# Performance work log

Measured on AMD Instinct MI355X. Metric: run time of the kernel, lower is better.

Reference implementation:

```python
import jax, jax.numpy as jnp
import numpy as np
import math

B, L, D_MODEL, H = 8, 3072, 1024, 16
E = D_MODEL // H                      # d_keys = d_values = 64
FACTOR = 1
TOP_K = int(FACTOR * math.log(L))     # = 8 delay taps


def setup_inputs() -> dict:
    key = jax.random.key(0)
    ks = jax.random.split(key, 11)
    s = 0.02
    return {
        "queries": jax.random.normal(ks[0], (B, L, D_MODEL), jnp.float32),
        "keys":    jax.random.normal(ks[1], (B, L, D_MODEL), jnp.float32),
        "values":  jax.random.normal(ks[2], (B, L, D_MODEL), jnp.float32),
        "Wq": jax.random.normal(ks[3], (D_MODEL, D_MODEL), jnp.float32) * s,
        "bq": jnp.zeros((D_MODEL,), jnp.float32),
        "Wk": jax.random.normal(ks[4], (D_MODEL, D_MODEL), jnp.float32) * s,
        "bk": jnp.zeros((D_MODEL,), jnp.float32),
        "Wv": jax.random.normal(ks[5], (D_MODEL, D_MODEL), jnp.float32) * s,
        "bv": jnp.zeros((D_MODEL,), jnp.float32),
        "Wo": jax.random.normal(ks[6], (D_MODEL, D_MODEL), jnp.float32) * s,
        "bo": jnp.zeros((D_MODEL,), jnp.float32),
    }


def reference(queries, keys, values, Wq, bq, Wk, bk, Wv, bv, Wo, bo):
    # Q/K/V projections -> [B, L, H, E]
    q = (queries @ Wq + bq).reshape(B, L, H, E)
    k = (keys    @ Wk + bk).reshape(B, L, H, E)
    v = (values  @ Wv + bv).reshape(B, L, H, E)

    # -> [B, H, E, L], correlate along time via FFT
    qh = q.transpose(0, 2, 3, 1)
    kh = k.transpose(0, 2, 3, 1)
    vh = v.transpose(0, 2, 3, 1)
    qf = jnp.fft.rfft(qh, axis=-1)
    kf = jnp.fft.rfft(kh, axis=-1)
    corr = jnp.fft.irfft(qf * jnp.conj(kf), n=L, axis=-1)  # [B, H, E, L]

    # per-batch top-k delay selection on head/channel-averaged correlation
    mean_value = corr.mean(axis=(1, 2))                    # [B, L]
    weights, delay = jax.lax.top_k(mean_value, TOP_K)      # [B, K]
    tmp_corr = jax.nn.softmax(weights, axis=-1)            # [B, K]

    # time-delay aggregation: circular gather per selected delay, weighted sum
    init_index = jnp.arange(L)
    agg = jnp.zeros_like(vh)
    for i in range(TOP_K):  # small static loop over top-k taps
        idx = (init_index[None, :] + delay[:, i:i + 1]) % L            # [B, L]
        idx4 = jnp.broadcast_to(idx[:, None, None, :], vh.shape)       # [B,H,E,L]
        pattern = jnp.take_along_axis(vh, idx4, axis=-1)
        agg = agg + pattern * tmp_corr[:, i][:, None, None, None]

    # back to [B, L, H*E], output projection
    V = agg.transpose(0, 3, 1, 2).reshape(B, L, H * E)
    return V @ Wo + bo
```

## Files before the change

kernel.cpp:

```cpp
#include <hip/hip_runtime.h>
#include <math.h>

#define BSZ 8
#define LEN 3072
#define DM 1024
#define TOPK 8

typedef __attribute__((ext_vector_type(8))) short short8;
typedef __attribute__((ext_vector_type(4))) float f32x4;

__device__ __forceinline__ unsigned short f2bf(float x) {
    unsigned int u = __builtin_bit_cast(unsigned int, x);
    u += 0x7fffu + ((u >> 16) & 1u);
    return (unsigned short)(u >> 16);
}
__device__ __forceinline__ float bf2f(unsigned short h) {
    unsigned int u = ((unsigned int)h) << 16;
    return __builtin_bit_cast(float, u);
}
__device__ __forceinline__ void gl_lds16(const void* g, void* l) {
    __builtin_amdgcn_global_load_lds(
        (const __attribute__((address_space(1))) unsigned int*)g,
        (__attribute__((address_space(3))) unsigned int*)l, 16, 0, 0);
}

#define GBM 128
#define GBN 128
#define GBK 16

__global__ __launch_bounds__(256) void gemm_f32_sk(const float* __restrict__ A,
    const float* __restrict__ B, float* __restrict__ P, int M, int N, int K)
{
    __shared__ float As[GBK][GBM];
    __shared__ float Bs[GBK][GBN];
    const int tid = threadIdx.x;
    const int tx = tid & 15, ty = tid >> 4;
    const size_t m0 = (size_t)blockIdx.y * GBM;
    const size_t n0 = (size_t)blockIdx.x * GBN;
    const int ksl = K >> 2;
    const int kb = blockIdx.z * ksl, ke = kb + ksl;
    const int arow = tid >> 2, acol = (tid & 3) << 2;
    const int brow = tid >> 5, bcol = (tid & 31) << 2;

    float acc[8][8];
#pragma unroll
    for (int i = 0; i < 8; i++)
#pragma unroll
        for (int j = 0; j < 8; j++) acc[i][j] = 0.f;

    const float* Ap0 = A + (m0 + arow) * (size_t)K + acol;
    const float* Ap1 = A + (m0 + arow + 64) * (size_t)K + acol;
    const float* Bp0 = B + (size_t)brow * N + n0 + bcol;
    const float* Bp1 = B + (size_t)(brow + 8) * N + n0 + bcol;

    for (int k0 = kb; k0 < ke; k0 += GBK) {
        float4 a0 = *(const float4*)(Ap0 + k0);
        float4 a1 = *(const float4*)(Ap1 + k0);
        float4 b0 = *(const float4*)(Bp0 + (size_t)k0 * N);
        float4 b1 = *(const float4*)(Bp1 + (size_t)k0 * N);
        __syncthreads();
        As[acol + 0][arow] = a0.x; As[acol + 1][arow] = a0.y;
        As[acol + 2][arow] = a0.z; As[acol + 3][arow] = a0.w;
        As[acol + 0][arow + 64] = a1.x; As[acol + 1][arow + 64] = a1.y;
        As[acol + 2][arow + 64] = a1.z; As[acol + 3][arow + 64] = a1.w;
        *(float4*)&Bs[brow][bcol] = b0;
        *(float4*)&Bs[brow + 8][bcol] = b1;
        __syncthreads();
#pragma unroll
        for (int kk = 0; kk < GBK; kk++) {
            float av[8], bv[8];
            *(float4*)&av[0] = *(const float4*)&As[kk][ty * 8];
            *(float4*)&av[4] = *(const float4*)&As[kk][ty * 8 + 4];
            *(float4*)&bv[0] = *(const float4*)&Bs[kk][tx * 8];
            *(float4*)&bv[4] = *(const float4*)&Bs[kk][tx * 8 + 4];
#pragma unroll
            for (int i = 0; i < 8; i++)
#pragma unroll
                for (int j = 0; j < 8; j++)
                    acc[i][j] = fmaf(av[i], bv[j], acc[i][j]);
        }
    }
    float* Pz = P + (size_t)blockIdx.z * M * N;
#pragma unroll
    for (int i = 0; i < 8; i++) {
        size_t row = m0 + (size_t)(ty * 8 + i);
        float* Cp = Pz + row * N + n0 + tx * 8;
#pragma unroll
        for (int j = 0; j < 8; j++) Cp[j] = acc[i][j];
    }
}

__global__ __launch_bounds__(256) void reduce4_f32(const float* __restrict__ P,
                                                   float* __restrict__ C, int n)
{
    int i = (blockIdx.x * 256 + threadIdx.x) * 4;
    if (i >= n) return;
    float4 a = *(const float4*)(P + i);
    float4 b = *(const float4*)(P + (size_t)n + i);
    float4 c = *(const float4*)(P + 2 * (size_t)n + i);
    float4 d = *(const float4*)(P + 3 * (size_t)n + i);
    float4 o = {a.x + b.x + c.x + d.x, a.y + b.y + c.y + d.y,
                a.z + b.z + c.z + d.z, a.w + b.w + c.w + d.w};
    *(float4*)(C + i) = o;
}

__device__ __forceinline__ void xcd_tile(int& bx, int& by) {
    int nbx = gridDim.x, nby = gridDim.y;
    int nwg = nbx * nby;
    int flat = by * nbx + bx;
    if (!(nwg & 7)) {
        int sw = (flat & 7) * (nwg >> 3) + (flat >> 3);
        bx = sw % nbx;
        by = sw / nbx;
    }
}

__global__ __launch_bounds__(256) void gemm_split_zT(
    const unsigned short* __restrict__ Khi, const unsigned short* __restrict__ Klo,
    const unsigned short* __restrict__ AhiT, const unsigned short* __restrict__ AloT,
    const float* __restrict__ bias, float* __restrict__ zT, int M, int N, int K)
{
    __shared__ unsigned short Ah[128 * 32];
    __shared__ unsigned short Al[128 * 32];
    __shared__ unsigned short Bh[128 * 32];
    __shared__ unsigned short Bl[128 * 32];
    const int tid = threadIdx.x;
    const int lane = tid & 63;
    const int wv = tid >> 6;
    const int wm = wv >> 1, wn = wv & 1;
    const int l16 = lane & 15, quad = lane >> 4;
    int bx = blockIdx.x, by = blockIdx.y;
    xcd_tile(bx, by);
    const size_t m0 = (size_t)by * 128;
    const size_t n0 = (size_t)bx * 128;

    const int s0 = tid, s1 = tid + 256;
    const size_t oA0 = (m0 + (s0 >> 2)) * (size_t)K + (s0 & 3) * 8;
    const size_t oA1 = (m0 + (s1 >> 2)) * (size_t)K + (s1 & 3) * 8;
    const size_t oB0 = (n0 + (s0 >> 2)) * (size_t)K + (s0 & 3) * 8;
    const size_t oB1 = (n0 + (s1 >> 2)) * (size_t)K + (s1 & 3) * 8;

    f32x4 acc[4][4];
#pragma unroll
    for (int i = 0; i < 4; i++)
#pragma unroll
        for (int j = 0; j < 4; j++) acc[i][j] = (f32x4){0.f, 0.f, 0.f, 0.f};

    for (int k0 = 0; k0 < K; k0 += 32) {
        __syncthreads();
        gl_lds16(Khi + oA0 + k0, &Ah[s0 * 8]);
        gl_lds16(Khi + oA1 + k0, &Ah[s1 * 8]);
        gl_lds16(Klo + oA0 + k0, &Al[s0 * 8]);
        gl_lds16(Klo + oA1 + k0, &Al[s1 * 8]);
        gl_lds16(AhiT + oB0 + k0, &Bh[s0 * 8]);
        gl_lds16(AhiT + oB1 + k0, &Bh[s1 * 8]);
        gl_lds16(AloT + oB0 + k0, &Bl[s0 * 8]);
        gl_lds16(AloT + oB1 + k0, &Bl[s1 * 8]);
        __syncthreads();
        short8 ah[4], al[4], bh[4], bl[4];
#pragma unroll
        for (int mi = 0; mi < 4; mi++) {
            int off = (wm * 64 + mi * 16 + l16) * 32 + quad * 8;
            ah[mi] = *(const short8*)&Ah[off];
            al[mi] = *(const short8*)&Al[off];
        }
#pragma unroll
        for (int ni = 0; ni < 4; ni++) {
            int off = (wn * 64 + ni * 16 + l16) * 32 + quad * 8;
            bh[ni] = *(const short8*)&Bh[off];
            bl[ni] = *(const short8*)&Bl[off];
        }
#pragma unroll
        for (int mi = 0; mi < 4; mi++)
#pragma unroll
            for (int ni = 0; ni < 4; ni++) {
                acc[mi][ni] = __builtin_amdgcn_mfma_f32_16x16x32_bf16(
                    ah[mi], bh[ni], acc[mi][ni], 0, 0, 0);
                acc[mi][ni] = __builtin_amdgcn_mfma_f32_16x16x32_bf16(
                    ah[mi], bl[ni], acc[mi][ni], 0, 0, 0);
                acc[mi][ni] = __builtin_amdgcn_mfma_f32_16x16x32_bf16(
                    al[mi], bh[ni], acc[mi][ni], 0, 0, 0);
            }
    }

    const int b = (int)(m0 / LEN);
    const int t0 = (int)(m0 % LEN);
#pragma unroll
    for (int mi = 0; mi < 4; mi++) {
#pragma unroll
        for (int ni = 0; ni < 4; ni++) {
            int c = (int)n0 + wn * 64 + ni * 16 + l16;
            int t = t0 + wm * 64 + mi * 16 + quad * 4;
            float bb = bias[c];
            float* zp = zT + ((size_t)b * DM + c) * LEN + t;
#pragma unroll
            for (int r = 0; r < 4; r++) zp[r] = acc[mi][ni][r] + bb;
        }
    }
}

__global__ __launch_bounds__(256) void gemm_bf16(const unsigned short* __restrict__ A,
    const unsigned short* __restrict__ Bt, const float* __restrict__ bias,
    void* __restrict__ C, int M, int N, int K, int cmode)
{
    __shared__ unsigned short As[128 * 32];
    __shared__ unsigned short Bs[128 * 32];
    const int tid = threadIdx.x;
    const int lane = tid & 63;
    const int wv = tid >> 6;
    const int wm = wv >> 1, wn = wv & 1;
    const int l16 = lane & 15, quad = lane >> 4;
    int bx = blockIdx.x, by = blockIdx.y;
    xcd_tile(bx, by);
    const size_t m0 = (size_t)by * 128;
    const size_t n0 = (size_t)bx * 128;

    const int s0 = tid, s1 = tid + 256;
    const unsigned short* gA0 = A + (m0 + (s0 >> 2)) * (size_t)K + (s0 & 3) * 8;
    const unsigned short* gA1 = A + (m0 + (s1 >> 2)) * (size_t)K + (s1 & 3) * 8;
    const unsigned short* gB0 = Bt + (n0 + (s0 >> 2)) * (size_t)K + (s0 & 3) * 8;
    const unsigned short* gB1 = Bt + (n0 + (s1 >> 2)) * (size_t)K + (s1 & 3) * 8;
    unsigned short* lA0 = &As[s0 * 8];
    unsigned short* lA1 = &As[s1 * 8];
    unsigned short* lB0 = &Bs[s0 * 8];
    unsigned short* lB1 = &Bs[s1 * 8];

    f32x4 acc[4][4];
#pragma unroll
    for (int i = 0; i < 4; i++)
#pragma unroll
        for (int j = 0; j < 4; j++) acc[i][j] = (f32x4){0.f, 0.f, 0.f, 0.f};

    for (int k0 = 0; k0 < K; k0 += 32) {
        __syncthreads();
        gl_lds16(gA0 + k0, lA0);
        gl_lds16(gA1 + k0, lA1);
        gl_lds16(gB0 + k0, lB0);
        gl_lds16(gB1 + k0, lB1);
        __syncthreads();
        short8 af[4], bf[4];
#pragma unroll
        for (int mi = 0; mi < 4; mi++)
            af[mi] = *(const short8*)&As[(wm * 64 + mi * 16 + l16) * 32 + quad * 8];
#pragma unroll
        for (int ni = 0; ni < 4; ni++)
            bf[ni] = *(const short8*)&Bs[(wn * 64 + ni * 16 + l16) * 32 + quad * 8];
#pragma unroll
        for (int mi = 0; mi < 4; mi++)
#pragma unroll
            for (int ni = 0; ni < 4; ni++)
                acc[mi][ni] = __builtin_amdgcn_mfma_f32_16x16x32_bf16(
                    af[mi], bf[ni], acc[mi][ni], 0, 0, 0);
    }

#pragma unroll
    for (int mi = 0; mi < 4; mi++) {
#pragma unroll
        for (int ni = 0; ni < 4; ni++) {
            int gm = (int)m0 + wm * 64 + mi * 16 + quad * 4;
            int gn = (int)n0 + wn * 64 + ni * 16 + l16;
            float bb = bias ? bias[gn] : 0.f;
#pragma unroll
            for (int r = 0; r < 4; r++) {
                float v = acc[mi][ni][r] + bb;
                if (cmode == 0)
                    ((float*)C)[(size_t)(gm + r) * N + gn] = v;
                else
                    ((unsigned short*)C)[(size_t)(gm + r) * N + gn] = f2bf(v);
            }
        }
    }
}

__global__ __launch_bounds__(256) void transpose_bld(const float* __restrict__ in,
                                                     float* __restrict__ out)
{
    __shared__ float tile[32][33];
    int b = blockIdx.z;
    int d0 = blockIdx.x * 32, t0 = blockIdx.y * 32;
    int tx = threadIdx.x & 31, ty = threadIdx.x >> 5;
    const float* ip = in + (size_t)b * LEN * DM;
    float* op = out + (size_t)b * DM * LEN;
#pragma unroll
    for (int r = 0; r < 4; r++)
        tile[ty * 4 + r][tx] = ip[(size_t)(t0 + ty * 4 + r) * DM + d0 + tx];
    __syncthreads();
#pragma unroll
    for (int r = 0; r < 4; r++)
        op[(size_t)(d0 + ty * 4 + r) * LEN + t0 + tx] = tile[tx][ty * 4 + r];
}

__global__ __launch_bounds__(256) void transpose_1024(const float* __restrict__ in,
                                                      float* __restrict__ out)
{
    __shared__ float tile[32][33];
    int bx = blockIdx.x & 31, by = blockIdx.x >> 5;
    int tx = threadIdx.x & 31, tq = threadIdx.x >> 5;
#pragma unroll
    for (int r = 0; r < 4; r++)
        tile[tq * 4 + r][tx] = in[(size_t)(by * 32 + tq * 4 + r) * 1024 + bx * 32 + tx];
    __syncthreads();
#pragma unroll
    for (int r = 0; r < 4; r++)
        out[(size_t)(bx * 32 + tq * 4 + r) * 1024 + by * 32 + tx] = tile[tx][tq * 4 + r];
}

__global__ __launch_bounds__(256) void transpose_w_bf16(const float* __restrict__ in,
                                                        unsigned short* __restrict__ out)
{
    __shared__ float tile[32][33];
    int bx = blockIdx.x & 31, by = blockIdx.x >> 5;
    int tx = threadIdx.x & 31, tq = threadIdx.x >> 5;
#pragma unroll
    for (int r = 0; r < 4; r++)
        tile[tq * 4 + r][tx] = in[(size_t)(by * 32 + tq * 4 + r) * 1024 + bx * 32 + tx];
    __syncthreads();
#pragma unroll
    for (int r = 0; r < 4; r++)
        out[(size_t)(bx * 32 + tq * 4 + r) * 1024 + by * 32 + tx] = f2bf(tile[tx][tq * 4 + r]);
}

__global__ __launch_bounds__(256) void transpose_w_split(const float* __restrict__ in,
    unsigned short* __restrict__ hi, unsigned short* __restrict__ lo)
{
    __shared__ float tile[32][33];
    int bx = blockIdx.x & 31, by = blockIdx.x >> 5;
    int tx = threadIdx.x & 31, tq = threadIdx.x >> 5;
#pragma unroll
    for (int r = 0; r < 4; r++)
        tile[tq * 4 + r][tx] = in[(size_t)(by * 32 + tq * 4 + r) * 1024 + bx * 32 + tx];
    __syncthreads();
#pragma unroll
    for (int r = 0; r < 4; r++) {
        float x = tile[tx][tq * 4 + r];
        unsigned short h = f2bf(x);
        unsigned short l = f2bf(x - bf2f(h));
        size_t o = (size_t)(bx * 32 + tq * 4 + r) * 1024 + by * 32 + tx;
        hi[o] = h; lo[o] = l;
    }
}

__global__ __launch_bounds__(256) void split_bf16(const float* __restrict__ in,
    unsigned short* __restrict__ hi, unsigned short* __restrict__ lo, size_t n)
{
    size_t i = ((size_t)blockIdx.x * 256 + threadIdx.x) * 4;
    if (i >= n) return;
    float4 v = *(const float4*)(in + i);
    ushort4 h, l;
    h.x = f2bf(v.x); l.x = f2bf(v.x - bf2f(h.x));
    h.y = f2bf(v.y); l.y = f2bf(v.y - bf2f(h.y));
    h.z = f2bf(v.z); l.z = f2bf(v.z - bf2f(h.z));
    h.w = f2bf(v.w); l.w = f2bf(v.w - bf2f(h.w));
    *(ushort4*)(hi + i) = h;
    *(ushort4*)(lo + i) = l;
}

__global__ __launch_bounds__(256) void conv_bf16(const float* __restrict__ in,
                                                 unsigned short* __restrict__ out, size_t n)
{
    size_t i = ((size_t)blockIdx.x * 256 + threadIdx.x) * 4;
    if (i >= n) return;
    float4 v = *(const float4*)(in + i);
    ushort4 o;
    o.x = f2bf(v.x); o.y = f2bf(v.y); o.z = f2bf(v.z); o.w = f2bf(v.w);
    *(ushort4*)(out + i) = o;
}

__global__ __launch_bounds__(256) void bz_kernel(const float* __restrict__ bk,
    const float* __restrict__ WqT, float* __restrict__ bz)
{
    int j = blockIdx.x * 256 + threadIdx.x;
    float s = 0.f;
    for (int d = 0; d < 1024; d++) s = fmaf(bk[d], WqT[(size_t)d * 1024 + j], s);
    bz[j] = s;
}

__device__ __forceinline__ int swz(int i) { return i ^ ((i >> 4) & 15); }

__device__ __forceinline__ float2 cmul(float2 a, float2 b) {
    return make_float2(a.x * b.x - a.y * b.y, a.x * b.y + a.y * b.x);
}

struct TwRegs {
    float2 wA[5], w2[5], w1[4], w2c[4];
};

__device__ __forceinline__ void make_tw(TwRegs& T, int tid)
{
    const float TWO_PI = 6.28318530717958647692f;
#pragma unroll
    for (int si = 0; si < 5; si++) {
        int s = si * 2;
        int a = (tid >> s) << s;
        float sv, cv; sincosf(-TWO_PI * (float)a / 1024.f, &sv, &cv);
        T.wA[si] = make_float2(cv, sv);
        T.w2[si] = make_float2(cv * cv - sv * sv, 2.f * cv * sv);
    }
#pragma unroll
    for (int j = 0; j < 4; j++) {
        int k2 = tid + (j << 8);
        float sv, cv; sincosf(-TWO_PI * (float)k2 / 3072.f, &sv, &cv);
        T.w1[j] = make_float2(cv, sv);
        T.w2c[j] = make_float2(cv * cv - sv * sv, 2.f * cv * sv);
    }
}

__device__ __forceinline__ void fft3072_r4(float2* __restrict__ bufA,
                                           float2* __restrict__ bufB,
                                           const TwRegs& T, int tid)
{
    float2* src = bufA;
    float2* dst = bufB;
#pragma unroll
    for (int s = 0; s < 10; s += 2) {
        const int st = 1 << s;
        const int q = tid & (st - 1);
        const int p = tid >> s;
        const float2 wA = T.wA[s >> 1];
        const float2 w2 = T.w2[s >> 1];
        const int io = q + (p << (s + 2));
#pragma unroll
        for (int k = 0; k < 3; k++) {
            const int base = k << 10;
            float2 a1 = src[swz(base + tid)];
            float2 a2 = src[swz(base + tid + 256)];
            float2 b1 = src[swz(base + tid + 512)];
            float2 b2 = src[swz(base + tid + 768)];
            float2 uA0 = make_float2(a1.x + b1.x, a1.y + b1.y);
            float2 d1  = make_float2(a1.x - b1.x, a1.y - b1.y);
            float2 uA1 = cmul(d1, wA);
            float2 uB0 = make_float2(a2.x + b2.x, a2.y + b2.y);
            float2 d2  = make_float2(a2.x - b2.x, a2.y - b2.y);
            float2 e   = cmul(d2, wA);
            float2 uB1 = make_float2(e.y, -e.x);
            float2 o0 = make_float2(uA0.x + uB0.x, uA0.y + uB0.y);
            float2 o1 = make_float2(uA1.x + uB1.x, uA1.y + uB1.y);
            float2 e2 = make_float2(uA0.x - uB0.x, uA0.y - uB0.y);
            float2 e3 = make_float2(uA1.x - uB1.x, uA1.y - uB1.y);
            dst[swz(base + io)] = o0;
            dst[swz(base + io + st)] = o1;
            dst[swz(base + io + 2 * st)] = cmul(e2, w2);
            dst[swz(base + io + 3 * st)] = cmul(e3, w2);
        }
        __syncthreads();
        float2* t = src; src = dst; dst = t;
    }
    const float OMR = -0.5f, OMI = -0.86602540378443864676f;
#pragma unroll
    for (int j = 0; j < 4; j++) {
        int k2 = tid + (j << 8);
        float2 y0 = src[swz(k2)];
        float2 y1 = src[swz(1024 + k2)];
        float2 y2 = src[swz(2048 + k2)];
        float2 w1 = T.w1[j];
        float2 w2c = T.w2c[j];
        float2 u1 = cmul(y1, w1);
        float2 u2 = cmul(y2, w2c);
        dst[swz(k2)] = make_float2(y0.x + u1.x + u2.x, y0.y + u1.y + u2.y);
        dst[swz(1024 + k2)] = make_float2(
            y0.x + (OMR * u1.x - OMI * u1.y) + (OMR * u2.x + OMI * u2.y),
            y0.y + (OMR * u1.y + OMI * u1.x) + (OMR * u2.y - OMI * u2.x));
        dst[swz(2048 + k2)] = make_float2(
            y0.x + (OMR * u1.x + OMI * u1.y) + (OMR * u2.x - OMI * u2.y),
            y0.y + (OMR * u1.y - OMI * u1.x) + (OMR * u2.y + OMI * u2.x));
    }
    __syncthreads();
}

#define SLAB 3104

__global__ __launch_bounds__(256) void fft_corr(const float* __restrict__ qT,
    const float* __restrict__ zT, float* __restrict__ Spart)
{
    __shared__ float2 bufA[3072], bufB[3072];
    const int tid = threadIdx.x;
    const int b = blockIdx.x >> 6;
    const int c0 = (blockIdx.x & 63) << 4;
    TwRegs T;
    make_tw(T, tid);
    float pR[6], pI[6];
#pragma unroll
    for (int j = 0; j < 6; j++) { pR[j] = 0.f; pI[j] = 0.f; }
    float eR = 0.f, eI = 0.f;

    const float* qp = qT + ((size_t)b * DM + c0) * LEN;
    const float* zp = zT + ((size_t)b * DM + c0) * LEN;
    float qv[12], zv[12];
#pragma unroll
    for (int j = 0; j < 12; j++) {
        int t = tid + (j << 8);
        qv[j] = qp[t]; zv[j] = zp[t];
    }

    for (int ci = 0; ci < 16; ci++) {
#pragma unroll
        for (int j = 0; j < 12; j++) {
            int t = tid + (j << 8);
            int t1 = t % 3, t2 = t / 3;
            bufA[swz(t1 * 1024 + t2)] = make_float2(qv[j], zv[j]);
        }
        if (ci < 15) {
            const float* qn = qp + (size_t)(ci + 1) * LEN;
            const float* zn = zp + (size_t)(ci + 1) * LEN;
#pragma unroll
            for (int j = 0; j < 12; j++) {
                int t = tid + (j << 8);
                qv[j] = qn[t]; zv[j] = zn[t];
            }
        }
        __syncthreads();
        fft3072_r4(bufA, bufB, T, tid);
#pragma unroll
        for (int j = 0; j < 6; j++) {
            int f = tid + (j << 8);
            int fc = (f == 0) ? 0 : 3072 - f;
            float2 Wf = bufA[swz(f)];
            float2 Wc = bufA[swz(fc)];
            float WcI = -Wc.y;
            float qR = 0.5f * (Wf.x + Wc.x), qI = 0.5f * (Wf.y + WcI);
            float dR = Wf.x - Wc.x, dI = Wf.y - WcI;
            float zR = 0.5f * dI, zI = -0.5f * dR;
            pR[j] += qR * zR + qI * zI;
            pI[j] += qI * zR - qR * zI;
        }
        if (tid == 0) {
            float2 Wf = bufA[swz(1536)];
            eR += Wf.x * Wf.y;
        }
        __syncthreads();
    }
    float2* Pb = (float2*)(Spart + (size_t)blockIdx.x * SLAB);
#pragma unroll
    for (int j = 0; j < 6; j++) {
        int f = tid + (j << 8);
        Pb[f] = make_float2(pR[j], pI[j]);
    }
    if (tid == 0) Pb[1536] = make_float2(eR, eI);
}

__global__ __launch_bounds__(256) void reduce_S(const float* __restrict__ Spart,
                                                float* __restrict__ S)
{
    int g = blockIdx.x * 256 + threadIdx.x;
    if (g >= BSZ * 3074) return;
    int b = g / 3074, r = g - b * 3074;
    const float* p = Spart + (size_t)(b * 64) * SLAB + r;
    float s = 0.f;
#pragma unroll 8
    for (int k = 0; k < 64; k++) s += p[(size_t)k * SLAB];
    S[(size_t)b * 6144 + r] = s;
}

__global__ __launch_bounds__(256) void ifft_mean(const float* __restrict__ S,
                                                 float* __restrict__ mv)
{
    __shared__ float2 bufA[3072], bufB[3072];
    const int tid = threadIdx.x;
    const int b = blockIdx.x;
    TwRegs T;
    make_tw(T, tid);
    for (int t = tid; t < 3072; t += 256) {
        int tt = (t <= 1536) ? t : 3072 - t;
        float sR = S[((size_t)b * 3072 + tt) * 2 + 0];
        float sI = S[((size_t)b * 3072 + tt) * 2 + 1];
        float im = (t > 1536) ? sI : -sI;
        int t1 = t % 3, t2 = t / 3;
        bufA[swz(t1 * 1024 + t2)] = make_float2(sR, im);
    }
    __syncthreads();
    fft3072_r4(bufA, bufB, T, tid);
    const float scale = 1.f / (3072.f * 1024.f);
    for (int t = tid; t < 3072; t += 256)
        mv[(size_t)b * 3072 + t] = bufA[swz(t)].x * scale;
}

__global__ __launch_bounds__(256) void topk_softmax(const float* __restrict__ mv,
    float* __restrict__ wout, int* __restrict__ dout)
{
    const int b = blockIdx.x, tid = threadIdx.x;
    __shared__ float v[3072];
    __shared__ float rv[256];
    __shared__ int   ri[256];
    __shared__ float topv[TOPK];
    __shared__ int   topi[TOPK];
    for (int t = tid; t < 3072; t += 256) v[t] = mv[(size_t)b * 3072 + t];
    __syncthreads();
    for (int it = 0; it < TOPK; it++) {
        float best = -3.0e38f; int bi = 0;
        for (int t = tid; t < 3072; t += 256) {
            float x = v[t];
            if (x > best) { best = x; bi = t; }
        }
        rv[tid] = best; ri[tid] = bi;
        __syncthreads();
        for (int off = 128; off > 0; off >>= 1) {
            if (tid < off) {
                float ov = rv[tid + off]; int oi = ri[tid + off];
                if (ov > rv[tid] || (ov == rv[tid] && oi < ri[tid])) {
                    rv[tid] = ov; ri[tid] = oi;
                }
            }
            __syncthreads();
        }
        if (tid == 0) { topv[it] = rv[0]; topi[it] = ri[0]; v[ri[0]] = -3.0e38f; }
        __syncthreads();
    }
    if (tid == 0) {
        float m = topv[0];
        float e[TOPK]; float ssum = 0.f;
        for (int i = 0; i < TOPK; i++) { e[i] = expf(topv[i] - m); ssum += e[i]; }
        for (int i = 0; i < TOPK; i++) {
            wout[b * TOPK + i] = e[i] / ssum;
            dout[b * TOPK + i] = topi[i];
        }
    }
}

__global__ __launch_bounds__(256) void agg_bf16(const unsigned short* __restrict__ V,
    const float* __restrict__ w, const int* __restrict__ d,
    unsigned short* __restrict__ agg)
{
    size_t gid = (size_t)blockIdx.x * 256 + threadIdx.x;
    int c8 = (int)(gid & 127);
    size_t rest = gid >> 7;
    int t = (int)(rest % LEN);
    int b = (int)(rest / LEN);
    float acc[8];
#pragma unroll
    for (int j = 0; j < 8; j++) acc[j] = 0.f;
#pragma unroll
    for (int i = 0; i < TOPK; i++) {
        float wi = w[b * TOPK + i];
        int r = t + d[b * TOPK + i];
        if (r >= LEN) r -= LEN;
        const unsigned short* vp = V + ((size_t)b * LEN + r) * DM + c8 * 8;
        uint4 raw = *(const uint4*)vp;
        unsigned int uu[4] = {raw.x, raw.y, raw.z, raw.w};
#pragma unroll
        for (int k = 0; k < 4; k++) {
            acc[2 * k]     = fmaf(wi, bf2f((unsigned short)(uu[k] & 0xffff)), acc[2 * k]);
            acc[2 * k + 1] = fmaf(wi, bf2f((unsigned short)(uu[k] >> 16)), acc[2 * k + 1]);
        }
    }
    unsigned int ou[4];
#pragma unroll
    for (int k = 0; k < 4; k++)
        ou[k] = (unsigned int)f2bf(acc[2 * k]) | ((unsigned int)f2bf(acc[2 * k + 1]) << 16);
    uint4 o = {ou[0], ou[1], ou[2], ou[3]};
    *(uint4*)(agg + gid * 8) = o;
}

extern "C" void kernel_launch(void* const* d_in, const int* in_sizes, int n_in,
                              void* d_out, int out_size, void* d_ws, size_t ws_size,
                              hipStream_t stream)
{
    const float* queries = (const float*)d_in[0];
    const float* keys    = (const float*)d_in[1];
    const float* values  = (const float*)d_in[2];
    const float* Wq = (const float*)d_in[3];
    const float* Wk = (const float*)d_in[5];
    const float* bk = (const float*)d_in[6];
    const float* Wv = (const float*)d_in[7];
    const float* bv = (const float*)d_in[8];
    const float* Wo = (const float*)d_in[9];
    const float* bo = (const float*)d_in[10];
    float* out = (float*)d_out;

    char* ws = (char*)d_ws;
    size_t off = 0;
    auto alloc = [&](size_t bytes) -> char* {
        char* p = ws + off;
        off += (bytes + 255) & ~(size_t)255;
        return p;
    };
    const size_t BLD = (size_t)BSZ * LEN * DM;
    float* WqT  = (float*)alloc((size_t)1024 * 1024 * 4);
    float* Amat = (float*)alloc((size_t)1024 * 1024 * 4);
    unsigned short* AhiT = (unsigned short*)alloc((size_t)1024 * 1024 * 2);
    unsigned short* AloT = (unsigned short*)alloc((size_t)1024 * 1024 * 2);
    float* bz   = (float*)alloc(1024 * 4);
    float* S    = (float*)alloc((size_t)BSZ * 3072 * 2 * 4);
    float* mv   = (float*)alloc((size_t)BSZ * 3072 * 4);
    float* wsm  = (float*)alloc(BSZ * TOPK * 4);
    int*   dly  = (int*)alloc(BSZ * TOPK * 4);
    unsigned short* WvT = (unsigned short*)alloc((size_t)1024 * 1024 * 2);
    unsigned short* WoT = (unsigned short*)alloc((size_t)1024 * 1024 * 2);
    char* bigA = alloc(BLD * 4);
    char* bigB = alloc(BLD * 4);
    unsigned short* khi = (unsigned short*)bigA;
    unsigned short* klo = (unsigned short*)(bigA + BLD * 2);
    float* qT = (float*)bigA;
    float* zT = (float*)bigB;
    float* Apart = (float*)bigB;
    unsigned short* vb16 = (unsigned short*)bigA;
    unsigned short* aggb = (unsigned short*)(bigA + BLD * 2);
    unsigned short* Vb   = (unsigned short*)bigB;
    float* Spart = WqT;

    const int BL = BSZ * LEN;

    transpose_1024<<<1024, 256, 0, stream>>>(Wq, WqT);
    gemm_f32_sk<<<dim3(8, 8, 4), 256, 0, stream>>>(Wk, WqT, Apart, 1024, 1024, 1024);
    reduce4_f32<<<1024, 256, 0, stream>>>(Apart, Amat, 1024 * 1024);
    bz_kernel<<<4, 256, 0, stream>>>(bk, WqT, bz);
    transpose_w_split<<<1024, 256, 0, stream>>>(Amat, AhiT, AloT);
    split_bf16<<<(int)((BLD / 4 + 255) / 256), 256, 0, stream>>>(keys, khi, klo, BLD);
    gemm_split_zT<<<dim3(8, 192), 256, 0, stream>>>(khi, klo, AhiT, AloT, bz, zT,
                                                    BL, 1024, 1024);
    transpose_bld<<<dim3(32, 96, 8), 256, 0, stream>>>(queries, qT);
    fft_corr<<<BSZ * 64, 256, 0, stream>>>(qT, zT, Spart);
    reduce_S<<<(BSZ * 3074 + 255) / 256, 256, 0, stream>>>(Spart, S);
    ifft_mean<<<BSZ, 256, 0, stream>>>(S, mv);
    topk_softmax<<<BSZ, 256, 0, stream>>>(mv, wsm, dly);

    conv_bf16<<<(int)((BLD / 4 + 255) / 256), 256, 0, stream>>>(values, vb16, BLD);
    transpose_w_bf16<<<1024, 256, 0, stream>>>(Wv, WvT);
    transpose_w_bf16<<<1024, 256, 0, stream>>>(Wo, WoT);
    gemm_bf16<<<dim3(8, 192), 256, 0, stream>>>(vb16, WvT, bv, Vb, BL, 1024, 1024, 1);
    agg_bf16<<<(int)(((size_t)BL * 128) / 256), 256, 0, stream>>>(Vb, wsm, dly, aggb);
    gemm_bf16<<<dim3(8, 192), 256, 0, stream>>>(aggb, WoT, bo, out, BL, 1024, 1024, 0);
}
```

Before: 891.1 us.

## Unify GEMMs into triple-buffered swizzled pipeline and rebalance FFT block split

Replaces the split-bf16 and plain bf16 GEMM kernels with one templated kernel that triple-buffers LDS tiles using async global-to-LDS loads. It waits on the vmcnt counter instead of issuing two full barriers per k-step, and XOR-swizzles the LDS layout to avoid bank conflicts. The split-precision GEMM is recast as three sequential K-phases (hi*hi, hi*lo, lo*hi) over the same pipeline. The FFT correlation work is also redistributed from 64 to 96 blocks per batch so more blocks fill the GPU, at the cost of more partial slabs for the reduction to sum.

```diff
diff --git a/kernel.cpp b/kernel.cpp
--- a/kernel.cpp
+++ b/kernel.cpp
@@ -115,15 +115,14 @@
     }
 }
 
-__global__ __launch_bounds__(256) void gemm_split_zT(
-    const unsigned short* __restrict__ Khi, const unsigned short* __restrict__ Klo,
-    const unsigned short* __restrict__ AhiT, const unsigned short* __restrict__ AloT,
-    const float* __restrict__ bias, float* __restrict__ zT, int M, int N, int K)
-{
-    __shared__ unsigned short Ah[128 * 32];
-    __shared__ unsigned short Al[128 * 32];
-    __shared__ unsigned short Bh[128 * 32];
-    __shared__ unsigned short Bl[128 * 32];
+template<int KMODE, int CMODE>
+__global__ __launch_bounds__(256, 3) void gemm_pipe(
+    const unsigned short* __restrict__ A0, const unsigned short* __restrict__ A1,
+    const unsigned short* __restrict__ B0, const unsigned short* __restrict__ B1,
+    const float* __restrict__ bias, void* __restrict__ C, int M, int N, int NT)
+{
+    __shared__ unsigned short Ab[3][128 * 32];
+    __shared__ unsigned short Bb[3][128 * 32];
     const int tid = threadIdx.x;
     const int lane = tid & 63;
     const int wv = tid >> 6;
@@ -135,10 +134,41 @@
     const size_t n0 = (size_t)bx * 128;
 
     const int s0 = tid, s1 = tid + 256;
-    const size_t oA0 = (m0 + (s0 >> 2)) * (size_t)K + (s0 & 3) * 8;
-    const size_t oA1 = (m0 + (s1 >> 2)) * (size_t)K + (s1 & 3) * 8;
-    const size_t oB0 = (n0 + (s0 >> 2)) * (size_t)K + (s0 & 3) * 8;
-    const size_t oB1 = (n0 + (s1 >> 2)) * (size_t)K + (s1 & 3) * 8;
+    const int g0 = ((s0 & 3) ^ ((s0 >> 3) & 3)) * 8;
+    const int g1 = ((s1 & 3) ^ ((s1 >> 3) & 3)) * 8;
+    const size_t oA0 = (m0 + (s0 >> 2)) * 1024 + g0;
+    const size_t oA1 = (m0 + (s1 >> 2)) * 1024 + g1;
+    const size_t oB0 = (n0 + (s0 >> 2)) * 1024 + g0;
+    const size_t oB1 = (n0 + (s1 >> 2)) * 1024 + g1;
+
+    int aoff[4], boff[4];
+#pragma unroll
+    for (int mi = 0; mi < 4; mi++) {
+        int row = wm * 64 + mi * 16 + l16;
+        aoff[mi] = row * 32 + ((quad ^ ((row >> 1) & 3)) << 3);
+    }
+#pragma unroll
+    for (int ni = 0; ni < 4; ni++) {
+        int row = wn * 64 + ni * 16 + l16;
+        boff[ni] = row * 32 + ((quad ^ ((row >> 1) & 3)) << 3);
+    }
+
+    auto stage = [&](int kt, int buf) {
+        const unsigned short *Asrc, *Bsrc;
+        int ko;
+        if (KMODE == 0) {
+            Asrc = A0; Bsrc = B0; ko = kt * 32;
+        } else {
+            int ks = kt >> 5;
+            Asrc = (ks < 2) ? A0 : A1;
+            Bsrc = (ks == 1) ? B1 : B0;
+            ko = (kt & 31) * 32;
+        }
+        gl_lds16(Asrc + oA0 + ko, &Ab[buf][s0 * 8]);
+        gl_lds16(Asrc + oA1 + ko, &Ab[buf][s1 * 8]);
+        gl_lds16(Bsrc + oB0 + ko, &Bb[buf][s0 * 8]);
+        gl_lds16(Bsrc + oB1 + ko, &Bb[buf][s1 * 8]);
+    };
 
     f32x4 acc[4][4];
 #pragma unroll
@@ -146,127 +176,69 @@
 #pragma unroll
         for (int j = 0; j < 4; j++) acc[i][j] = (f32x4){0.f, 0.f, 0.f, 0.f};
 
-    for (int k0 = 0; k0 < K; k0 += 32) {
-        __syncthreads();
-        gl_lds16(Khi + oA0 + k0, &Ah[s0 * 8]);
-        gl_lds16(Khi + oA1 + k0, &Ah[s1 * 8]);
-        gl_lds16(Klo + oA0 + k0, &Al[s0 * 8]);
-        gl_lds16(Klo + oA1 + k0, &Al[s1 * 8]);
-        gl_lds16(AhiT + oB0 + k0, &Bh[s0 * 8]);
-        gl_lds16(AhiT + oB1 + k0, &Bh[s1 * 8]);
-        gl_lds16(AloT + oB0 + k0, &Bl[s0 * 8]);
-        gl_lds16(AloT + oB1 + k0, &Bl[s1 * 8]);
-        __syncthreads();
-        short8 ah[4], al[4], bh[4], bl[4];
-#pragma unroll
-        for (int mi = 0; mi < 4; mi++) {
-            int off = (wm * 64 + mi * 16 + l16) * 32 + quad * 8;
-            ah[mi] = *(const short8*)&Ah[off];
-            al[mi] = *(const short8*)&Al[off];
-        }
-#pragma unroll
-        for (int ni = 0; ni < 4; ni++) {
-            int off = (wn * 64 + ni * 16 + l16) * 32 + quad * 8;
-            bh[ni] = *(const short8*)&Bh[off];
-            bl[ni] = *(const short8*)&Bl[off];
-        }
+    stage(0, 0);
+    stage(1, 1);
+    asm volatile("s_waitcnt vmcnt(4)\n\ts_barrier" ::: "memory");
+
+    int cur = 0;
+    for (int kt = 0; kt < NT; ++kt) {
+        int sb = cur - 1; if (sb < 0) sb = 2;
+        if (kt + 2 < NT) stage(kt + 2, sb);
+        short8 af[4], bf[4];
 #pragma unroll
         for (int mi = 0; mi < 4; mi++)
-#pragma unroll
-            for (int ni = 0; ni < 4; ni++) {
-                acc[mi][ni] = __builtin_amdgcn_mfma_f32_16x16x32_bf16(
-                    ah[mi], bh[ni], acc[mi][ni], 0, 0, 0);
-                acc[mi][ni] = __builtin_amdgcn_mfma_f32_16x16x32_bf16(
-                    ah[mi], bl[ni], acc[mi][ni], 0, 0, 0);
-                acc[mi][ni] = __builtin_amdgcn_mfma_f32_16x16x32_bf16(
-                    al[mi], bh[ni], acc[mi][ni], 0, 0, 0);
-            }
-    }
-
-    const int b = (int)(m0 / LEN);
-    const int t0 = (int)(m0 % LEN);
-#pragma unroll
-    for (int mi = 0; mi < 4; mi++) {
-#pragma unroll
-        for (int ni = 0; ni < 4; ni++) {
-            int c = (int)n0 + wn * 64 + ni * 16 + l16;
-            int t = t0 + wm * 64 + mi * 16 + quad * 4;
-            float bb = bias[c];
-            float* zp = zT + ((size_t)b * DM + c) * LEN + t;
-#pragma unroll
-            for (int r = 0; r < 4; r++) zp[r] = acc[mi][ni][r] + bb;
-        }
-    }
-}
-
-__global__ __launch_bounds__(256) void gemm_bf16(const unsigned short* __restrict__ A,
-    const unsigned short* __restrict__ Bt, const float* __restrict__ bias,
-    void* __restrict__ C, int M, int N, int K, int cmode)
-{
-    __shared__ unsigned short As[128 * 32];
-    __shared__ unsigned short Bs[128 * 32];
-    const int tid = threadIdx.x;
-    const int lane = tid & 63;
-    const int wv = tid >> 6;
-    const int wm = wv >> 1, wn = wv & 1;
-    const int l16 = lane & 15, quad = lane >> 4;
-    int bx = blockIdx.x, by = blockIdx.y;
-    xcd_tile(bx, by);
-    const size_t m0 = (size_t)by * 128;
-    const size_t n0 = (size_t)bx * 128;
-
-    const int s0 = tid, s1 = tid + 256;
-    const unsigned short* gA0 = A + (m0 + (s0 >> 2)) * (size_t)K + (s0 & 3) * 8;
-    const unsigned short* gA1 = A + (m0 + (s1 >> 2)) * (size_t)K + (s1 & 3) * 8;
-    const unsigned short* gB0 = Bt + (n0 + (s0 >> 2)) * (size_t)K + (s0 & 3) * 8;
-    const unsigned short* gB1 = Bt + (n0 + (s1 >> 2)) * (size_t)K + (s1 & 3) * 8;
-    unsigned short* lA0 = &As[s0 * 8];
-    unsigned short* lA1 = &As[s1 * 8];
-    unsigned short* lB0 = &Bs[s0 * 8];
-    unsigned short* lB1 = &Bs[s1 * 8];
-
-    f32x4 acc[4][4];
-#pragma unroll
-    for (int i = 0; i < 4; i++)
-#pragma unroll
-        for (int j = 0; j < 4; j++) acc[i][j] = (f32x4){0.f, 0.f, 0.f, 0.f};
-
-    for (int k0 = 0; k0 < K; k0 += 32) {
-        __syncthreads();
-        gl_lds16(gA0 + k0, lA0);
-        gl_lds16(gA1 + k0, lA1);
-        gl_lds16(gB0 + k0, lB0);
-        gl_lds16(gB1 + k0, lB1);
-        __syncthreads();
-        short8 af[4], bf[4];
-#pragma unroll
-        for (int mi = 0; mi < 4; mi++)
-            af[mi] = *(const short8*)&As[(wm * 64 + mi * 16 + l16) * 32 + quad * 8];
+            af[mi] = *(const short8*)&Ab[cur][aoff[mi]];
 #pragma unroll
         for (int ni = 0; ni < 4; ni++)
-            bf[ni] = *(const short8*)&Bs[(wn * 64 + ni * 16 + l16) * 32 + quad * 8];
+            bf[ni] = *(const short8*)&Bb[cur][boff[ni]];
+        __builtin_amdgcn_s_setprio(1);
 #pragma unroll
         for (int mi = 0; mi < 4; mi++)
 #pragma unroll
             for (int ni = 0; ni < 4; ni++)
                 acc[mi][ni] = __builtin_amdgcn_mfma_f32_16x16x32_bf16(
                     af[mi], bf[ni], acc[mi][ni], 0, 0, 0);
-    }
-
-#pragma unroll
-    for (int mi = 0; mi < 4; mi++) {
-#pragma unroll
-        for (int ni = 0; ni < 4; ni++) {
-            int gm = (int)m0 + wm * 64 + mi * 16 + quad * 4;
-            int gn = (int)n0 + wn * 64 + ni * 16 + l16;
-            float bb = bias ? bias[gn] : 0.f;
-#pragma unroll
-            for (int r = 0; r < 4; r++) {
-                float v = acc[mi][ni][r] + bb;
-                if (cmode == 0)
-                    ((float*)C)[(size_t)(gm + r) * N + gn] = v;
-                else
-                    ((unsigned short*)C)[(size_t)(gm + r) * N + gn] = f2bf(v);
+        __builtin_amdgcn_s_setprio(0);
+        if (kt + 1 < NT) {
+            if (kt + 2 < NT)
+                asm volatile("s_waitcnt vmcnt(4)\n\ts_barrier" ::: "memory");
+            else
+                asm volatile("s_waitcnt vmcnt(0)\n\ts_barrier" ::: "memory");
+        }
+        cur = (cur == 2) ? 0 : cur + 1;
+    }
+
+    if (CMODE == 2) {
+        const int b = (int)(m0 / LEN);
+        const int t0 = (int)(m0 % LEN);
+#pragma unroll
+        for (int mi = 0; mi < 4; mi++) {
+#pragma unroll
+            for (int ni = 0; ni < 4; ni++) {
+                int c = (int)n0 + wn * 64 + ni * 16 + l16;
+                int t = t0 + wm * 64 + mi * 16 + quad * 4;
+                float bb = bias[c];
+                float* zp = (float*)C + ((size_t)b * DM + c) * LEN + t;
+#pragma unroll
+                for (int r = 0; r < 4; r++) zp[r] = acc[mi][ni][r] + bb;
+            }
+        }
+    } else {
+#pragma unroll
+        for (int mi = 0; mi < 4; mi++) {
+#pragma unroll
+            for (int ni = 0; ni < 4; ni++) {
+                int gm = (int)m0 + wm * 64 + mi * 16 + quad * 4;
+                int gn = (int)n0 + wn * 64 + ni * 16 + l16;
+                float bb = bias[gn];
+#pragma unroll
+                for (int r = 0; r < 4; r++) {
+                    float v = acc[mi][ni][r] + bb;
+                    if (CMODE == 0)
+                        ((float*)C)[(size_t)(gm + r) * N + gn] = v;
+                    else
+                        ((unsigned short*)C)[(size_t)(gm + r) * N + gn] = f2bf(v);
+                }
             }
         }
     }
@@ -468,14 +440,17 @@
 }
 
 #define SLAB 3104
+#define FFTBPB 96
 
 __global__ __launch_bounds__(256) void fft_corr(const float* __restrict__ qT,
     const float* __restrict__ zT, float* __restrict__ Spart)
 {
     __shared__ float2 bufA[3072], bufB[3072];
     const int tid = threadIdx.x;
-    const int b = blockIdx.x >> 6;
-    const int c0 = (blockIdx.x & 63) << 4;
+    const int b = blockIdx.x / FFTBPB;
+    const int g = blockIdx.x % FFTBPB;
+    const int c0 = g * 10 + (g < 64 ? g : 64);
+    const int nch = (g < 64) ? 11 : 10;
     TwRegs T;
     make_tw(T, tid);
     float pR[6], pI[6];
@@ -492,14 +467,14 @@
         qv[j] = qp[t]; zv[j] = zp[t];
     }
 
-    for (int ci = 0; ci < 16; ci++) {
+    for (int ci = 0; ci < nch; ci++) {
 #pragma unroll
         for (int j = 0; j < 12; j++) {
             int t = tid + (j << 8);
             int t1 = t % 3, t2 = t / 3;
             bufA[swz(t1 * 1024 + t2)] = make_float2(qv[j], zv[j]);
         }
-        if (ci < 15) {
+        if (ci + 1 < nch) {
             const float* qn = qp + (size_t)(ci + 1) * LEN;
             const float* zn = zp + (size_t)(ci + 1) * LEN;
 #pragma unroll
@@ -544,10 +519,10 @@
     int g = blockIdx.x * 256 + threadIdx.x;
     if (g >= BSZ * 3074) return;
     int b = g / 3074, r = g - b * 3074;
-    const float* p = Spart + (size_t)(b * 64) * SLAB + r;
+    const float* p = Spart + (size_t)(b * FFTBPB) * SLAB + r;
     float s = 0.f;
 #pragma unroll 8
-    for (int k = 0; k < 64; k++) s += p[(size_t)k * SLAB];
+    for (int k = 0; k < FFTBPB; k++) s += p[(size_t)k * SLAB];
     S[(size_t)b * 6144 + r] = s;
 }
 
@@ -705,10 +680,10 @@
     bz_kernel<<<4, 256, 0, stream>>>(bk, WqT, bz);
     transpose_w_split<<<1024, 256, 0, stream>>>(Amat, AhiT, AloT);
     split_bf16<<<(int)((BLD / 4 + 255) / 256), 256, 0, stream>>>(keys, khi, klo, BLD);
-    gemm_split_zT<<<dim3(8, 192), 256, 0, stream>>>(khi, klo, AhiT, AloT, bz, zT,
-                                                    BL, 1024, 1024);
+    gemm_pipe<1, 2><<<dim3(8, 192), 256, 0, stream>>>(khi, klo, AhiT, AloT, bz, zT,
+                                                      BL, 1024, 96);
     transpose_bld<<<dim3(32, 96, 8), 256, 0, stream>>>(queries, qT);
-    fft_corr<<<BSZ * 64, 256, 0, stream>>>(qT, zT, Spart);
+    fft_corr<<<BSZ * FFTBPB, 256, 0, stream>>>(qT, zT, Spart);
     reduce_S<<<(BSZ * 3074 + 255) / 256, 256, 0, stream>>>(Spart, S);
     ifft_mean<<<BSZ, 256, 0, stream>>>(S, mv);
     topk_softmax<<<BSZ, 256, 0, stream>>>(mv, wsm, dly);
@@ -716,7 +691,9 @@
     conv_bf16<<<(int)((BLD / 4 + 255) / 256), 256, 0, stream>>>(values, vb16, BLD);
     transpose_w_bf16<<<1024, 256, 0, stream>>>(Wv, WvT);
     transpose_w_bf16<<<1024, 256, 0, stream>>>(Wo, WoT);
-    gemm_bf16<<<dim3(8, 192), 256, 0, stream>>>(vb16, WvT, bv, Vb, BL, 1024, 1024, 1);
+    gemm_pipe<0, 1><<<dim3(8, 192), 256, 0, stream>>>(vb16, nullptr, WvT, nullptr,
+                                                      bv, Vb, BL, 1024, 32);
     agg_bf16<<<(int)(((size_t)BL * 128) / 256), 256, 0, stream>>>(Vb, wsm, dly, aggb);
-    gemm_bf16<<<dim3(8, 192), 256, 0, stream>>>(aggb, WoT, bo, out, BL, 1024, 1024, 0);
-}
+    gemm_pipe<0, 0><<<dim3(8, 192), 256, 0, stream>>>(aggb, nullptr, WoT, nullptr,
+                                                      bo, out, BL, 1024, 32);
+}
```

Measured after the change: 901.3 us. No clear change (+1.2%).
